# Optimization experiments

Hardware: AMD Instinct MI355X
Metric: run time of the kernel (lower is better)

The kernel has to match this reference:

```python
import jax, jax.numpy as jnp
import numpy as np

B = 2        # batch items (row splits of length B+1)
NP = 16384   # points per batch item
NQ = 8192    # queries per batch item
K = 16       # neighbors


def setup_inputs() -> dict:
    key = jax.random.key(0)
    kp, kq = jax.random.split(key)
    points = jax.random.normal(kp, (B * NP, 3), dtype=jnp.float32)
    queries = jax.random.normal(kq, (B * NQ, 3), dtype=jnp.float32)
    points_row_splits = jnp.arange(B + 1, dtype=jnp.int32) * NP
    queries_row_splits = jnp.arange(B + 1, dtype=jnp.int32) * NQ
    return {
        "points": points,
        "queries": queries,
        "k": K,
        "points_row_splits": points_row_splits,
        "queries_row_splits": queries_row_splits,
    }


def reference(points, queries, k, points_row_splits, queries_row_splits):
    """Batched KNN search, metric='L2' (squared distances),
    ignore_query_point=False, return_distances=True.

    Equal-size row splits -> view the ragged batch as dense [B, N, 3].
    Returns (neighbors_index, neighbors_row_splits, neighbors_distance)
    matching Open3D's compact layout: every query has exactly k neighbors
    (k <= points per batch item), so neighbors_row_splits = arange(M+1)*k.
    Indices are global into the flat `points` tensor.
    """
    b = points_row_splits.shape[0] - 1
    npb = points.shape[0] // b   # points per batch item
    nqb = queries.shape[0] // b  # queries per batch item
    P = points.reshape(b, npb, 3)
    Q = queries.reshape(b, nqb, 3)

    # squared L2 distances: [b, nqb, npb]
    d = (jnp.sum(Q * Q, axis=-1)[:, :, None]
         + jnp.sum(P * P, axis=-1)[:, None, :]
         - 2.0 * jnp.einsum('bqd,bpd->bqp', Q, P))

    neg_d, idx = jax.lax.top_k(-d, k)          # smallest-k distances
    dist = jnp.maximum(-neg_d, 0.0)            # clamp tiny negatives

    # local per-batch indices -> global indices into flat points
    gidx = idx + (jnp.arange(b, dtype=idx.dtype) * npb)[:, None, None]

    neighbors_index = gidx.reshape(-1)
    neighbors_row_splits = jnp.arange(b * nqb + 1, dtype=jnp.int32) * k
    neighbors_distance = dist.reshape(-1)
    return neighbors_index, neighbors_row_splits, neighbors_distance
```

## Files before the change

### kernel.cpp

```cpp
#include <hip/hip_runtime.h>

#define NP_   16384
#define NQ_   8192
#define NB_   2
#define K_    16
#define TPB   256
#define PTPB  1024

#define GD    20
#define G3    (GD*GD*GD)
#define ORG   (-4.25f)
#define W     (8.5f / 20.0f)
#define INVW  (20.0f / 8.5f)

#define IDX_OFF 0
#define RS_OFF  (NB_*NQ_*K_)
#define RS_N    (NB_*NQ_+1)
#define DST_OFF (RS_OFF + RS_N)

typedef unsigned long long ull;
typedef float f32x2 __attribute__((ext_vector_type(2)));

__device__ __forceinline__ int mbcnt64(ull m) {
    return __builtin_amdgcn_mbcnt_hi((unsigned)(m >> 32),
           __builtin_amdgcn_mbcnt_lo((unsigned)m, 0));
}

__device__ __forceinline__ int cell_of(float x, float y, float z) {
    int ix = (int)floorf((x - ORG) * INVW); ix = min(max(ix, 0), GD-1);
    int iy = (int)floorf((y - ORG) * INVW); iy = min(max(iy, 0), GD-1);
    int iz = (int)floorf((z - ORG) * INVW); iz = min(max(iz, 0), GD-1);
    return (ix*GD + iy)*GD + iz;
}

__global__ void knn_hist(const float* __restrict__ pts, int* __restrict__ counts) {
    int i = blockIdx.x*TPB + threadIdx.x;
    if (i < NB_*NP_) {
        int b = i >> 14;
        int cid = cell_of(pts[i*3], pts[i*3+1], pts[i*3+2]);
        atomicAdd(&counts[b*(G3+1) + cid], 1);
    }
}

__global__ __launch_bounds__(PTPB) void knn_prefix(int* __restrict__ counts,
                                                   int* __restrict__ cursors) {
    const int CPT = (G3 + PTPB - 1) / PTPB;
    int b = blockIdx.x, tid = threadIdx.x;
    int lane = tid & 63, w = tid >> 6;
    int* cnt = counts + b*(G3+1);
    int base = tid * CPT;
    int tsum = 0;
    for (int j = 0; j < CPT; ++j) { int ix = base+j; if (ix < G3) tsum += cnt[ix]; }
    int v = tsum;
    #pragma unroll
    for (int off = 1; off < 64; off <<= 1) {
        int t = __shfl_up(v, off);
        if (lane >= off) v += t;
    }
    __shared__ int wsum[PTPB/64];
    if (lane == 63) wsum[w] = v;
    __syncthreads();
    int wbase = 0;
    for (int k = 0; k < w; ++k) wbase += wsum[k];
    int run = wbase + v - tsum;
    for (int j = 0; j < CPT; ++j) {
        int ix = base+j;
        if (ix < G3) {
            int c = cnt[ix];
            cnt[ix] = run;
            cursors[b*G3 + ix] = run;
            run += c;
        }
    }
    if (tid == PTPB-1) cnt[G3] = run;
}

__global__ void knn_scatter(const float* __restrict__ pts, int* __restrict__ cursors,
                            float4* __restrict__ sorted) {
    int i = blockIdx.x*TPB + threadIdx.x;
    if (i < NB_*NP_) {
        int b = i >> 14, loc = i & (NP_-1);
        float x = pts[i*3], y = pts[i*3+1], z = pts[i*3+2];
        int cid = cell_of(x, y, z);
        int pos = atomicAdd(&cursors[b*G3 + cid], 1);
        sorted[(size_t)b*NP_ + pos] = make_float4(x, y, z, __int_as_float(loc));
    }
}

__global__ __launch_bounds__(TPB, 6) void knn_search(
        const float* __restrict__ qrs,
        const int* __restrict__ starts,
        const float4* __restrict__ sorted,
        float* __restrict__ out)
{
    #pragma clang fp contract(off)
    __shared__ float2 buf[4][128];

    const int tid  = threadIdx.x;
    const int lane = tid & 63;
    const int wv   = tid >> 6;
    const int gq   = blockIdx.x*4 + wv;
    const int batch = gq >> 13;
    const int gofs  = batch * NP_;
    const int sb    = batch * (G3+1);
    const float4* spts = sorted + (size_t)batch * NP_;

    const float qx = qrs[gq*3+0], qy = qrs[gq*3+1], qz = qrs[gq*3+2];
    const float sq = qx*qx + qy*qy + qz*qz;

    int cx = (int)floorf((qx - ORG) * INVW); cx = min(max(cx,0), GD-1);
    int cy = (int)floorf((qy - ORG) * INVW); cy = min(max(cy,0), GD-1);
    int cz = (int)floorf((qz - ORG) * INVW); cz = min(max(cz,0), GD-1);

    const float INF = __int_as_float(0x7f800000);
    float md = INF; int mi = 0x7fffffff;
    float th = INF;
    int cnt = 0;

    auto drain = [&]() {
        int rounds = (cnt + 63) >> 6;
        for (int r = 0; r < rounds; ++r) {
            int pos = (r << 6) + lane;
            float nd = INF; int ni = 0x7fffffff;
            if (pos < cnt) { float2 e = buf[wv][pos]; nd = e.x; ni = __float_as_int(e.y); }
            #pragma unroll
            for (int m = 2; m <= 64; m <<= 1) {
                #pragma unroll
                for (int j = m >> 1; j >= 1; j >>= 1) {
                    float od = __shfl_xor(nd, j);
                    int   oi = __shfl_xor(ni, j);
                    bool pl = (od < nd) || (od == nd && oi < ni);
                    bool keepmin = ((lane & j) == 0) == ((lane & m) == 0);
                    if (keepmin == pl) { nd = od; ni = oi; }
                }
            }
            float cd = __shfl(nd, 15 - (lane & 15));
            int   ci = __shfl(ni, 15 - (lane & 15));
            bool take = (cd < md) || (cd == md && ci < mi);
            if (take) { md = cd; mi = ci; }
            #pragma unroll
            for (int j = 8; j >= 1; j >>= 1) {
                float od = __shfl_xor(md, j, 16);
                int   oi = __shfl_xor(mi, j, 16);
                bool pl = (od < md) || (od == md && oi < mi);
                if ((((lane & 15) & j) == 0) == pl) { md = od; mi = oi; }
            }
        }
        cnt = 0;
        th = __shfl(md, 15);
    };

    auto process = [&](float4 p, bool act) {
        float d = INF; int idx = 0x7fffffff;
        if (act) {
            float spw = p.x*p.x + p.y*p.y + p.z*p.z;
            float ip = fmaf(p.z, qz, fmaf(p.y, qy, __fmul_rn(p.x, qx)));
            d = fmaf(-2.0f, ip, sq + spw);
            idx = __float_as_int(p.w);
        }
        bool pass = act && (d <= th);
        ull mk = __ballot(pass);
        if (mk) {
            int sl = cnt + mbcnt64(mk);
            if (pass) buf[wv][sl] = make_float2(d, __int_as_float(idx));
            cnt += (int)__popcll(mk);
            if (cnt >= 64) drain();
        }
    };

    {
        int cid0 = (cx*GD + cy)*GD + cz;
        int st0 = starts[sb + cid0];
        int n0  = starts[sb + cid0 + 1] - st0;
        for (int b0 = 0; b0 < n0; b0 += 64) {
            int o = b0 + lane;
            bool act = o < n0;
            float4 p = make_float4(0,0,0,0);
            if (act) p = spts[st0 + o];
            process(p, act);
        }
        if (cnt > 0) drain();
    }

    for (int R = 1; R <= GD; ++R) {
        const int S = 2*R + 1;
        const int F = S*S;
        const int lat = 4*(S-1);
        const int total = (R == 1) ? 27 : (2*F + (S-2)*lat);

        for (int cb = 0; cb < total; cb += 64) {
            int cidx = cb + lane;
            int n = 0, st = 0;
            if (cidx < total) {
                int di, dj, dk;
                if (R == 1) {
                    di = cidx/9 - 1; int r9 = cidx - (cidx/9)*9;
                    dj = r9/3 - 1;   dk = r9 - (r9/3)*3 - 1;
                } else if (cidx < F) {
                    di = -R; int t = cidx; int q = t/S; dj = q - R; dk = t - q*S - R;
                } else if (cidx < 2*F) {
                    di =  R; int t = cidx - F; int q = t/S; dj = q - R; dk = t - q*S - R;
                } else {
                    int t = cidx - 2*F;
                    int layer = t/lat; int pos = t - layer*lat;
                    di = layer + 1 - R;
                    int side = pos/(S-1); int u = pos - side*(S-1);
                    if      (side == 0) { dj = -R;     dk = -R + u; }
                    else if (side == 1) { dj = -R + u; dk =  R;     }
                    else if (side == 2) { dj =  R;     dk =  R - u; }
                    else                { dj =  R - u; dk = -R;     }
                }
                bool own = (di == 0) && (dj == 0) && (dk == 0);
                int ii = cx+di, jj = cy+dj, kk = cz+dk;
                if (!own && ii>=0 && jj>=0 && kk>=0 && ii<GD && jj<GD && kk<GD) {
                    float lox = ORG + (float)ii * W;
                    float loy = ORG + (float)jj * W;
                    float loz = ORG + (float)kk * W;
                    float dx = fmaxf(0.0f, fmaxf(lox - qx, qx - (lox + W)));
                    float dy = fmaxf(0.0f, fmaxf(loy - qy, qy - (loy + W)));
                    float dz = fmaxf(0.0f, fmaxf(loz - qz, qz - (loz + W)));
                    float mind2 = dx*dx + dy*dy + dz*dz;
                    if (mind2 <= th + 1e-3f) {
                        int cid = (ii*GD + jj)*GD + kk;
                        st = starts[sb + cid];
                        n  = starts[sb + cid + 1] - st;
                    }
                }
            }
            int pex = n;
            #pragma unroll
            for (int off = 1; off < 64; off <<= 1) {
                int t2 = __shfl_up(pex, off);
                if (lane >= off) pex += t2;
            }
            int T = __shfl(pex, 63);
            pex -= n;
            if (T == 0) continue;

            auto fetchB = [&](int bb, float4& p, bool& act) {
                int sI = bb + lane;
                int lo = 0;
                #pragma unroll
                for (int j = 32; j >= 1; j >>= 1) {
                    int m = lo + j;
                    int pv = __shfl(pex, m);
                    if (pv <= sI) lo = m;
                }
                int stL = __shfl(st, lo);
                int pL  = __shfl(pex, lo);
                act = sI < T;
                if (act) p = spts[stL + (sI - pL)];
            };

            float4 pA = make_float4(0,0,0,0), pB = make_float4(0,0,0,0);
            bool aA = false, aB = false;
            fetchB(0, pA, aA);
            if (64 < T) fetchB(64, pB, aB);
            for (int bb = 0; bb < T; bb += 64) {
                float4 pN = make_float4(0,0,0,0); bool aN = false;
                if (bb + 128 < T) fetchB(bb + 128, pN, aN);
                process(pA, aA);
                pA = pB; aA = aB;
                pB = pN; aB = aN;
            }
        }
        if (cnt > 0) drain();
        float bd = INF;
        if (cx - R > 0)      bd = fminf(bd, qx - (ORG + (float)(cx - R) * W));
        if (cx + R < GD - 1) bd = fminf(bd, (ORG + (float)(cx + R + 1) * W) - qx);
        if (cy - R > 0)      bd = fminf(bd, qy - (ORG + (float)(cy - R) * W));
        if (cy + R < GD - 1) bd = fminf(bd, (ORG + (float)(cy + R + 1) * W) - qy);
        if (cz - R > 0)      bd = fminf(bd, qz - (ORG + (float)(cz - R) * W));
        if (cz + R < GD - 1) bd = fminf(bd, (ORG + (float)(cz + R + 1) * W) - qz);
        if (bd * bd > th + 1e-3f) break;
    }
    drain();

    if (lane < K_) {
        out[IDX_OFF + gq*K_ + lane] = (float)(mi + gofs);
        out[DST_OFF + gq*K_ + lane] = fmaxf(md, 0.0f);
    }
    int gt = blockIdx.x*TPB + tid;
    if (gt < RS_N) out[RS_OFF + gt] = (float)(gt * K_);
}

#define QPB   16
#define TILE  1024
#define NTILES (NP_/TILE)
#define GPT   (TILE/64)
#define CBUF  80

__global__ __launch_bounds__(TPB, 4) void knn_fallback(const float* __restrict__ pts,
                                                       const float* __restrict__ qrs,
                                                       float* __restrict__ out)
{
    #pragma clang fp contract(off)
    __shared__ float4 tile[TILE];
    __shared__ float2 buf[QPB][CBUF];
    const int tid  = threadIdx.x;
    const int lane = tid & 63;
    const int s    = lane & 15;
    const int g    = lane >> 4;
    const int bq   = tid >> 4;
    const int gq   = blockIdx.x * QPB + bq;
    const int batch = gq >> 13;
    const int gofs  = batch * NP_;
    const float* pb = pts + (size_t)gofs * 3;
    const int qb   = (tid >> 6) << 2;
    float qxv[4], qyv[4], qzv[4], sqv[4];
    #pragma unroll
    for (int qi = 0; qi < 4; ++qi) {
        const float* qp = qrs + (size_t)(blockIdx.x * QPB + qb + qi) * 3;
        qxv[qi] = qp[0]; qyv[qi] = qp[1]; qzv[qi] = qp[2];
        sqv[qi] = qxv[qi]*qxv[qi] + qyv[qi]*qyv[qi] + qzv[qi]*qzv[qi];
    }
    const f32x2 qx01 = {qxv[0], qxv[1]}, qx23 = {qxv[2], qxv[3]};
    const f32x2 qy01 = {qyv[0], qyv[1]}, qy23 = {qyv[2], qyv[3]};
    const f32x2 qz01 = {qzv[0], qzv[1]}, qz23 = {qzv[2], qzv[3]};
    const f32x2 sq01 = {sqv[0], sqv[1]}, sq23 = {sqv[2], sqv[3]};
    const f32x2 n2   = {-2.0f, -2.0f};
    const float INF = __int_as_float(0x7f800000);
    float hd = INF; int hi = 0x7fffffff;
    float th0 = INF, th1 = INF, th2 = INF, th3 = INF;
    int cnt0 = 0, cnt1 = 0, cnt2 = 0, cnt3 = 0;
    auto drain = [&]() {
        int cmax = max(max(cnt0, cnt1), max(cnt2, cnt3));
        int mycnt = (g==0) ? cnt0 : (g==1) ? cnt1 : (g==2) ? cnt2 : cnt3;
        for (int r = 0; r < cmax; r += K_) {
            float nd = INF; int ni = 0x7fffffff;
            int pos = r + s;
            if (pos < mycnt) { float2 e = buf[bq][pos]; nd = e.x; ni = __float_as_int(e.y); }
            #pragma unroll
            for (int m = 2; m <= 16; m <<= 1) {
                #pragma unroll
                for (int j = m >> 1; j > 0; j >>= 1) {
                    float od = __shfl_xor(nd, j);
                    int   oi = __shfl_xor(ni, j);
                    bool pl = (od < nd) || (od == nd && oi < ni);
                    bool keepmin = ((s & j) == 0) == ((s & m) == 0);
                    if (keepmin == pl) { nd = od; ni = oi; }
                }
            }
            float od = __shfl_xor(nd, 15);
            int   oi = __shfl_xor(ni, 15);
            bool pl = (od < hd) || (od == hd && oi < hi);
            if (pl) { hd = od; hi = oi; }
            #pragma unroll
            for (int j = 8; j > 0; j >>= 1) {
                float od2 = __shfl_xor(hd, j);
                int   oi2 = __shfl_xor(hi, j);
                bool pl2 = (od2 < hd) || (od2 == hd && oi2 < hi);
                if (((s & j) == 0) == pl2) { hd = od2; hi = oi2; }
            }
        }
        cnt0 = cnt1 = cnt2 = cnt3 = 0;
        th0 = __shfl(hd, 15, 64); th1 = __shfl(hd, 31, 64);
        th2 = __shfl(hd, 47, 64); th3 = __shfl(hd, 63, 64);
    };
    for (int t = 0; t < NTILES; ++t) {
        __syncthreads();
        #pragma unroll
        for (int k = 0; k < TILE/TPB; ++k) {
            int lp = tid + k*TPB; int gp = t*TILE + lp;
            float x = pb[gp*3+0], y = pb[gp*3+1], z = pb[gp*3+2];
            float sp = x*x + y*y + z*z;
            tile[lp] = make_float4(x, y, z, sp);
        }
        __syncthreads();
        #pragma unroll 4
        for (int gi = 0; gi < GPT; ++gi) {
            float4 p = tile[gi*64 + lane];
            f32x2 x2 = {p.x, p.x}, y2 = {p.y, p.y}, z2 = {p.z, p.z};
            f32x2 sps = {p.w, p.w};
            f32x2 ip01 = __builtin_elementwise_fma(z2, qz01,
                         __builtin_elementwise_fma(y2, qy01, x2*qx01));
            f32x2 ip23 = __builtin_elementwise_fma(z2, qz23,
                         __builtin_elementwise_fma(y2, qy23, x2*qx23));
            f32x2 d01 = __builtin_elementwise_fma(n2, ip01, sq01 + sps);
            f32x2 d23 = __builtin_elementwise_fma(n2, ip23, sq23 + sps);
            float d0 = d01.x, d1 = d01.y, d2 = d23.x, d3 = d23.y;
            ull m0 = __ballot(d0 <= th0);
            ull m1 = __ballot(d1 <= th1);
            ull m2 = __ballot(d2 <= th2);
            ull m3 = __ballot(d3 <= th3);
            if (m0 | m1 | m2 | m3) {
                const float fpid = __int_as_float(t*TILE + gi*64 + lane);
                if (m0) { int sl = cnt0 + mbcnt64(m0);
                    if (d0 <= th0) buf[qb+0][sl] = make_float2(d0, fpid);
                    cnt0 += (int)__popcll(m0); }
                if (m1) { int sl = cnt1 + mbcnt64(m1);
                    if (d1 <= th1) buf[qb+1][sl] = make_float2(d1, fpid);
                    cnt1 += (int)__popcll(m1); }
                if (m2) { int sl = cnt2 + mbcnt64(m2);
                    if (d2 <= th2) buf[qb+2][sl] = make_float2(d2, fpid);
                    cnt2 += (int)__popcll(m2); }
                if (m3) { int sl = cnt3 + mbcnt64(m3);
                    if (d3 <= th3) buf[qb+3][sl] = make_float2(d3, fpid);
                    cnt3 += (int)__popcll(m3); }
                if ((cnt0 | cnt1 | cnt2 | cnt3) >= K_) drain();
            }
        }
    }
    drain();
    out[IDX_OFF + gq*K_ + s] = (float)(hi + gofs);
    out[DST_OFF + gq*K_ + s] = fmaxf(hd, 0.0f);
    int gt = blockIdx.x * TPB + tid;
    if (gt < RS_N) out[RS_OFF + gt] = (float)(gt * K_);
}

extern "C" void kernel_launch(void* const* d_in, const int* in_sizes, int n_in,
                              void* d_out, int out_size, void* d_ws, size_t ws_size,
                              hipStream_t stream)
{
    const float* pts = (const float*)d_in[0];
    const float* qrs = (const float*)d_in[1];
    float* out = (float*)d_out;
    (void)in_sizes; (void)n_in; (void)out_size;

    const size_t counts_ints = (size_t)NB_*(G3+1);
    const size_t cursor_ints = (size_t)NB_*G3;
    const size_t sort_off = ((counts_ints + cursor_ints)*4 + 15) & ~(size_t)15;
    const size_t need = sort_off + sizeof(float4)*(size_t)NB_*NP_;

    if (d_ws != nullptr && ws_size >= need) {
        int* counts  = (int*)d_ws;
        int* cursors = counts + counts_ints;
        float4* sorted = (float4*)((char*)d_ws + sort_off);
        hipMemsetAsync(counts, 0, counts_ints*sizeof(int), stream);
        knn_hist   <<<(NB_*NP_ + TPB-1)/TPB, TPB, 0, stream>>>(pts, counts);
        knn_prefix <<<NB_, PTPB, 0, stream>>>(counts, cursors);
        knn_scatter<<<(NB_*NP_ + TPB-1)/TPB, TPB, 0, stream>>>(pts, cursors, sorted);
        knn_search <<<NB_*NQ_/4, TPB, 0, stream>>>(qrs, counts, sorted, out);
    } else {
        knn_fallback<<<NB_*NQ_/QPB, TPB, 0, stream>>>(pts, qrs, out);
    }
}
```

Measured before the change: 98.57 us.

## Fuse grid histogram, prefix scan and scatter into one shared-memory build kernel

Replaces the memset plus three build kernels (histogram, prefix, scatter) with a single kernel per batch that counts cells with LDS atomics, scans in shared memory, and scatters points using LDS cursors. This removes several launches and global atomics along with the separate cursor array. In exchange, the build now runs on only two workgroups, so the point loop is serialized across 1024 threads per batch. The G3 ints of LDS (about 32KB) also limit occupancy.

```diff
diff --git a/kernel.cpp b/kernel.cpp
--- a/kernel.cpp
+++ b/kernel.cpp
@@ -33,57 +33,57 @@
     return (ix*GD + iy)*GD + iz;
 }
 
-__global__ void knn_hist(const float* __restrict__ pts, int* __restrict__ counts) {
-    int i = blockIdx.x*TPB + threadIdx.x;
-    if (i < NB_*NP_) {
-        int b = i >> 14;
-        int cid = cell_of(pts[i*3], pts[i*3+1], pts[i*3+2]);
-        atomicAdd(&counts[b*(G3+1) + cid], 1);
-    }
-}
-
-__global__ __launch_bounds__(PTPB) void knn_prefix(int* __restrict__ counts,
-                                                   int* __restrict__ cursors) {
+__global__ __launch_bounds__(PTPB) void knn_build(const float* __restrict__ pts,
+                                                  int* __restrict__ counts,
+                                                  float4* __restrict__ sorted) {
+    __shared__ int lcnt[G3];
+    __shared__ int wsum[PTPB/64];
+    const int b = blockIdx.x, tid = threadIdx.x;
+    const int lane = tid & 63, w = tid >> 6;
+    int* cg = counts + b*(G3+1);
+
+    for (int i = tid; i < G3; i += PTPB) lcnt[i] = 0;
+    __syncthreads();
+
+    for (int i = tid; i < NP_; i += PTPB) {
+        int gi = b*NP_ + i;
+        atomicAdd(&lcnt[cell_of(pts[gi*3], pts[gi*3+1], pts[gi*3+2])], 1);
+    }
+    __syncthreads();
+
     const int CPT = (G3 + PTPB - 1) / PTPB;
-    int b = blockIdx.x, tid = threadIdx.x;
-    int lane = tid & 63, w = tid >> 6;
-    int* cnt = counts + b*(G3+1);
     int base = tid * CPT;
     int tsum = 0;
-    for (int j = 0; j < CPT; ++j) { int ix = base+j; if (ix < G3) tsum += cnt[ix]; }
+    for (int j = 0; j < CPT; ++j) { int ix = base+j; if (ix < G3) tsum += lcnt[ix]; }
     int v = tsum;
     #pragma unroll
     for (int off = 1; off < 64; off <<= 1) {
         int t = __shfl_up(v, off);
         if (lane >= off) v += t;
     }
-    __shared__ int wsum[PTPB/64];
     if (lane == 63) wsum[w] = v;
     __syncthreads();
     int wbase = 0;
     for (int k = 0; k < w; ++k) wbase += wsum[k];
     int run = wbase + v - tsum;
+    __syncthreads();
     for (int j = 0; j < CPT; ++j) {
         int ix = base+j;
         if (ix < G3) {
-            int c = cnt[ix];
-            cnt[ix] = run;
-            cursors[b*G3 + ix] = run;
+            int c = lcnt[ix];
+            lcnt[ix] = run;
+            cg[ix] = run;
             run += c;
         }
     }
-    if (tid == PTPB-1) cnt[G3] = run;
-}
-
-__global__ void knn_scatter(const float* __restrict__ pts, int* __restrict__ cursors,
-                            float4* __restrict__ sorted) {
-    int i = blockIdx.x*TPB + threadIdx.x;
-    if (i < NB_*NP_) {
-        int b = i >> 14, loc = i & (NP_-1);
-        float x = pts[i*3], y = pts[i*3+1], z = pts[i*3+2];
-        int cid = cell_of(x, y, z);
-        int pos = atomicAdd(&cursors[b*G3 + cid], 1);
-        sorted[(size_t)b*NP_ + pos] = make_float4(x, y, z, __int_as_float(loc));
+    if (tid == PTPB-1) cg[G3] = run;
+    __syncthreads();
+
+    for (int i = tid; i < NP_; i += PTPB) {
+        int gi = b*NP_ + i;
+        float x = pts[gi*3], y = pts[gi*3+1], z = pts[gi*3+2];
+        int pos = atomicAdd(&lcnt[cell_of(x, y, z)], 1);
+        sorted[(size_t)b*NP_ + pos] = make_float4(x, y, z, __int_as_float(i));
     }
 }
 
@@ -418,19 +418,14 @@
     (void)in_sizes; (void)n_in; (void)out_size;
 
     const size_t counts_ints = (size_t)NB_*(G3+1);
-    const size_t cursor_ints = (size_t)NB_*G3;
-    const size_t sort_off = ((counts_ints + cursor_ints)*4 + 15) & ~(size_t)15;
+    const size_t sort_off = (counts_ints*4 + 15) & ~(size_t)15;
     const size_t need = sort_off + sizeof(float4)*(size_t)NB_*NP_;
 
     if (d_ws != nullptr && ws_size >= need) {
         int* counts  = (int*)d_ws;
-        int* cursors = counts + counts_ints;
         float4* sorted = (float4*)((char*)d_ws + sort_off);
-        hipMemsetAsync(counts, 0, counts_ints*sizeof(int), stream);
-        knn_hist   <<<(NB_*NP_ + TPB-1)/TPB, TPB, 0, stream>>>(pts, counts);
-        knn_prefix <<<NB_, PTPB, 0, stream>>>(counts, cursors);
-        knn_scatter<<<(NB_*NP_ + TPB-1)/TPB, TPB, 0, stream>>>(pts, cursors, sorted);
-        knn_search <<<NB_*NQ_/4, TPB, 0, stream>>>(qrs, counts, sorted, out);
+        knn_build <<<NB_, PTPB, 0, stream>>>(pts, counts, sorted);
+        knn_search<<<NB_*NQ_/4, TPB, 0, stream>>>(qrs, counts, sorted, out);
     } else {
         knn_fallback<<<NB_*NQ_/QPB, TPB, 0, stream>>>(pts, qrs, out);
     }
```

Result: faster. 87.09 us (-11.6%).
